# Performance work log

Hardware: AMD Instinct MI355X
Metric: run time of the kernel (lower is better)

## Reference

```python
import jax, jax.numpy as jnp
import numpy as np

B, L, D = 4, 2048, 64
N_HEAD = 4
LOCALITY = 0.2
PI = 3.141592653589793


def setup_inputs() -> dict:
    key = jax.random.key(0)
    k1, k2, k3 = jax.random.split(key, 3)
    mesh = jax.random.uniform(k1, (B, L, 2), dtype=jnp.float32)
    inputs = jax.random.normal(k2, (B, L, D), dtype=jnp.float32)
    lmda = jax.random.uniform(k3, (N_HEAD, 1, 1), dtype=jnp.float32)
    return {"mesh": mesh, "inputs": inputs, "lmda": lmda}


def reference(mesh, inputs, lmda):
    FMAX = jnp.finfo(jnp.float32).max
    # pairwise squared distances: (B, L, L)
    diff = mesh[:, :, None, :] - mesh[:, None, :, :]
    m_dist = jnp.sum(diff * diff, axis=-1)
    # per-head scale in (0, inf): tan(pi/4 * (1-eps) * (1 + sin(lmda)))
    scale = jnp.tan(0.25 * PI * (1.0 - 1e-07) * (1.0 + jnp.sin(lmda)))  # (H,1,1)
    scaled = m_dist[:, None, :, :] * scale  # (B, H, L, L)
    # row-wise quantile threshold (linear interpolation, matching torch.quantile)
    thresh = jnp.quantile(scaled, LOCALITY, axis=-1, keepdims=True)  # (B,H,L,1)
    masked = jnp.where(scaled <= thresh, scaled, FMAX)
    att = jax.nn.softmax(-masked, axis=-1)  # (B, H, L, L)
    # aggregate: (B,H,L,L) x (B,L,D) -> (B,L,H,D) -> (B,L,H*D)
    conv = jnp.einsum('bhnj,bjd->bnhd', att, inputs)
    conv = conv.reshape(inputs.shape[0], -1, N_HEAD * inputs.shape[-1])
    return jnp.concatenate([inputs, conv], axis=-1)
```

## Files before the change

kernel.cpp:

```cpp
#include <hip/hip_runtime.h>
#include <math.h>

#ifndef M_PI
#define M_PI 3.14159265358979323846
#endif

namespace {
constexpr int B_ = 4;
constexpr int L_ = 2048;
constexpr int D_ = 64;
constexpr int H_ = 4;
constexpr int RB = 8;
constexpr int KT = 64;
constexpr int NTILE = L_ / KT;
constexpr int CAPC = 256;
constexpr int OUTW = D_ + H_ * D_;
}

typedef __attribute__((ext_vector_type(8))) short bf16x8;
typedef __attribute__((ext_vector_type(4))) float f32x4;

__device__ __forceinline__ unsigned bf16_rne(float x) {
    unsigned u = __float_as_uint(x);
    return (u + 0x7fffu + ((u >> 16) & 1u)) >> 16;
}

__device__ __forceinline__ unsigned cvt_pk_bf16(float lo, float hi) {
    unsigned r;
    asm("v_cvt_pk_bf16_f32 %0, %1, %2" : "=v"(r) : "v"(lo), "v"(hi));
    return r;
}

#if defined(__has_builtin)
#if __has_builtin(__builtin_amdgcn_exp2f)
#define EXP2F(x) __builtin_amdgcn_exp2f(x)
#endif
#endif
#ifndef EXP2F
#define EXP2F(x) __expf((x) * 0.69314718055994531f)
#endif

#define LDS_FENCE() __builtin_amdgcn_s_waitcnt(0xC07F)

__global__ __launch_bounds__(256) void prep_thresh_kernel(
    const float* __restrict__ mesh,
    const float* __restrict__ inputs,
    char* __restrict__ ws,
    float* __restrict__ out)
{
    __shared__ unsigned s_hist[4][256];
    __shared__ float s_cand[4][256];

    const int t = threadIdx.x;
    const int l = t & 63;
    const int w = t >> 6;
    const int blk = blockIdx.x;

    if (t < 128) {
        const unsigned u = (unsigned)blk * 128u + (unsigned)t;
        const int pb = u >> 16;
        const int rem = u & 65535;
        const int tile = rem >> 12;
        const int idx = rem & 4095;
        const int n = idx & 63;
        const int kl = (idx >> 6) << 1;
        const float* inb = inputs + ((size_t)pb * L_ + tile * 128) * D_;
        char* wsb = ws + (size_t)pb * (L_ * D_ * 2) + tile * (128 * D_ * 2);
        const float x0 = inb[kl * D_ + n];
        const float x1 = inb[(kl + 1) * D_ + n];
        const int chunk = (kl >> 3) * 64 + n;
        const int e = kl & 7;
        *reinterpret_cast<unsigned*>(wsb + chunk * 16 + e * 2) =
            bf16_rne(x0) | (bf16_rne(x1) << 16);
    }

    const int row = blk * 4 + w;
    const int b = row >> 11;
    const int rl = row & 2047;
    const float2* meshg = reinterpret_cast<const float2*>(mesh) + (size_t)b * L_;
    unsigned* hw = s_hist[w];
    float* cw = s_cand[w];
    const float2 me = meshg[rl];

    *reinterpret_cast<uint4*>(&hw[l * 4]) = make_uint4(0u, 0u, 0u, 0u);
    LDS_FENCE();
    #pragma unroll 4
    for (int it = 0; it < 32; ++it) {
        const int j = (it << 6) + l;
        const float2 mj = meshg[j];
        const float dx = __fsub_rn(me.x, mj.x);
        const float dy = __fsub_rn(me.y, mj.y);
        const float d = __fadd_rn(__fmul_rn(dx, dx), __fmul_rn(dy, dy));
        int bin = (int)(d * 128.0f); bin = bin < 255 ? bin : 255;
        atomicAdd(&hw[bin], 1u);
    }
    LDS_FENCE();
    int lo, hi; unsigned base;
    {
        const uint4 hv = *reinterpret_cast<const uint4*>(&hw[l * 4]);
        const unsigned p0 = hv.x, p1 = p0 + hv.y, p2 = p1 + hv.z, p3 = p2 + hv.w;
        unsigned sc = p3;
        #pragma unroll
        for (int off = 1; off < 64; off <<= 1) {
            const unsigned uu = __shfl_up(sc, off);
            if (l >= off) sc += uu;
        }
        const unsigned eb = sc - p3;
        const unsigned cum[4] = {eb + p0, eb + p1, eb + p2, eb + p3};
        int flo = -1, fhi = -1; unsigned fbase = 0u;
        #pragma unroll
        for (int e = 0; e < 4; ++e) {
            const unsigned prev = e ? cum[e - 1] : eb;
            if (cum[e] > 409u && prev <= 409u) { flo = l * 4 + e; fbase = prev; }
            if (cum[e] > 410u && prev <= 410u) { fhi = l * 4 + e; }
        }
        const unsigned long long bmlo = __ballot(flo >= 0);
        const int srclo = (int)__builtin_ctzll(bmlo);
        lo = __shfl(flo, srclo);
        base = __shfl(fbase, srclo);
        const unsigned long long bmhi = __ballot(fhi >= 0);
        hi = __shfl(fhi, (int)__builtin_ctzll(bmhi));
    }
    unsigned cbase = 0u;
    #pragma unroll 4
    for (int it = 0; it < 32; ++it) {
        const int j = (it << 6) + l;
        const float2 mj = meshg[j];
        const float dx = __fsub_rn(me.x, mj.x);
        const float dy = __fsub_rn(me.y, mj.y);
        const float d = __fadd_rn(__fmul_rn(dx, dx), __fmul_rn(dy, dy));
        int bin = (int)(d * 128.0f); bin = bin < 255 ? bin : 255;
        const bool pred = (bin >= lo && bin <= hi);
        const unsigned long long bm = __ballot(pred);
        if (pred) {
            const unsigned p = cbase + (unsigned)__popcll(bm & ((1ull << l) - 1ull));
            if (p < (unsigned)CAPC) cw[p] = d;
        }
        cbase += (unsigned)__popcll(bm);
    }
    LDS_FENCE();
    const int m = (int)min(cbase, (unsigned)CAPC);
    const unsigned k409 = 409u - base;
    const unsigned k410 = 410u - base;
    const float lo_edge = (float)lo * 0.0078125f;
    const float sc2 = 32768.0f / (float)(hi - lo + 1);
    *reinterpret_cast<uint4*>(&hw[l * 4]) = make_uint4(0u, 0u, 0u, 0u);
    LDS_FENCE();
    #pragma unroll 2
    for (int ci = l; ci < m; ci += 64) {
        const float v = cw[ci];
        int b2 = (int)(__fmul_rn(__fsub_rn(v, lo_edge), sc2));
        b2 = b2 < 255 ? b2 : 255; b2 = b2 > 0 ? b2 : 0;
        atomicAdd(&hw[b2], 1u);
    }
    LDS_FENCE();
    int lo2, hi2; unsigned base2;
    {
        const uint4 hv = *reinterpret_cast<const uint4*>(&hw[l * 4]);
        const unsigned p0 = hv.x, p1 = p0 + hv.y, p2 = p1 + hv.z, p3 = p2 + hv.w;
        unsigned sc = p3;
        #pragma unroll
        for (int off = 1; off < 64; off <<= 1) {
            const unsigned uu = __shfl_up(sc, off);
            if (l >= off) sc += uu;
        }
        const unsigned eb = sc - p3;
        const unsigned cum[4] = {eb + p0, eb + p1, eb + p2, eb + p3};
        int flo = -1, fhi = -1; unsigned fbase = 0u;
        #pragma unroll
        for (int e = 0; e < 4; ++e) {
            const unsigned prev = e ? cum[e - 1] : eb;
            if (cum[e] > k409 && prev <= k409) { flo = l * 4 + e; fbase = prev; }
            if (cum[e] > k410 && prev <= k410) { fhi = l * 4 + e; }
        }
        const unsigned long long bmlo = __ballot(flo >= 0);
        const int srclo = (int)__builtin_ctzll(bmlo);
        lo2 = __shfl(flo, srclo);
        base2 = __shfl(fbase, srclo);
        const unsigned long long bmhi = __ballot(fhi >= 0);
        hi2 = __shfl(fhi, (int)__builtin_ctzll(bmhi));
    }
    float* c2 = reinterpret_cast<float*>(hw);
    unsigned cnt2 = 0u;
    for (int c0 = 0; c0 < m; c0 += 64) {
        const int ci = c0 + l;
        float v = 0.0f; bool pred = false;
        if (ci < m) {
            v = cw[ci];
            int b2 = (int)(__fmul_rn(__fsub_rn(v, lo_edge), sc2));
            b2 = b2 < 255 ? b2 : 255; b2 = b2 > 0 ? b2 : 0;
            pred = (b2 >= lo2 && b2 <= hi2);
        }
        const unsigned long long bm = __ballot(pred);
        if (pred) {
            const unsigned p = cnt2 + (unsigned)__popcll(bm & ((1ull << l) - 1ull));
            if (p < 256u) c2[p] = v;
        }
        cnt2 += (unsigned)__popcll(bm);
    }
    LDS_FENCE();
    const int c = (int)min(cnt2, 256u);
    const int q409 = (int)(k409 - base2);
    const int q410 = (int)(k410 - base2);
    if (l == 0) { cw[0] = 0.0f; cw[1] = 0.0f; }
    LDS_FENCE();
    #pragma unroll 1
    for (int cc0 = 0; cc0 < c; cc0 += 64) {
        const int ci = cc0 + l;
        const float v = (ci < c) ? c2[ci] : 0.0f;
        int lt = 0, le = 0;
        #pragma unroll 4
        for (int i = 0; i < c; ++i) {
            const float u = c2[i];
            lt += (u < v) ? 1 : 0;
            le += (u <= v) ? 1 : 0;
        }
        if (ci < c) {
            if (lt <= q409 && q409 < le) cw[0] = v;
            if (lt <= q410 && q410 < le) cw[1] = v;
        }
    }
    LDS_FENCE();
    if (l == 0) {
        const float d409 = cw[0], d410 = cw[1];
        const float pos = 0.2f * 2047.0f;
        const float g = pos - 409.0f;
        const float lw = 1.0f - g;
        const float thD = __fadd_rn(__fmul_rn(d409, lw), __fmul_rn(d410, g));
        out[(size_t)(b * L_ + rl) * OUTW + 319] = thD;
    }
}

__global__ __launch_bounds__(256, 4) void posatt_kernel(
    const float* __restrict__ mesh,
    const float* __restrict__ inputs,
    const float* __restrict__ lmda,
    const char* __restrict__ ws,
    float* __restrict__ out)
{
    __shared__ float s_C[32 * 64];
    __shared__ float s_scale[H_];
    __shared__ float s_thD[RB];
    __shared__ float s_ws2[2][2][16];

    const int t = threadIdx.x;
    const int l = t & 63;
    const int w = t >> 6;
    const int p_w  = w >> 1;
    const int ks_w = w & 1;

    const int blk = blockIdx.x;
    const int xcd = blk & 7;
    const int b = xcd >> 1;
    const int n0 = (((xcd & 1) << 7) + (blk >> 3)) * RB;

    const float2* meshg = reinterpret_cast<const float2*>(mesh) + (size_t)b * L_;

    if (t < H_) {
        const double lam = (double)lmda[t];
        const float C = (float)(0.25 * M_PI * (1.0 - 1e-07));
        const float s1 = (float)sin(lam);
        const float arg = __fmul_rn(C, __fadd_rn(1.0f, s1));
        s_scale[t] = (float)tan((double)arg);
    }
    if (t < RB) {
        s_thD[t] = out[(size_t)(b * L_ + n0 + t) * OUTW + 319];
    }
    __syncthreads();

    const int row16 = l & 15;
    const int kq = l >> 4;
    const int rl = row16 & 7;
    const float2 me = meshg[n0 + rl];
    const float thD = s_thD[rl];
    constexpr float LOG2E = 1.4426950408889634f;
    const float cH = __fmul_rn(-LOG2E, s_scale[p_w * 2 + (row16 >> 3)]);

    const char* bptr = ws + (size_t)b * (L_ * D_ * 2)
                     + ((size_t)(((ks_w * 4 + kq) * 64) + row16) << 4);
    const float4* mptr = reinterpret_cast<const float4*>(meshg) + (ks_w * 16 + kq * 4);

    f32x4 acc[4];
    acc[0] = (f32x4)0.0f; acc[1] = (f32x4)0.0f;
    acc[2] = (f32x4)0.0f; acc[3] = (f32x4)0.0f;
    float wacc = 0.0f;

    uint4 cb0, cb1, cb2, cb3;
    float4 cm0, cm1, cm2, cm3;
    auto LOADT = [&](int tl, uint4& B0, uint4& B1, uint4& B2, uint4& B3,
                     float4& M0, float4& M1, float4& M2, float4& M3) {
        const char* p = bptr + ((size_t)tl << 13);
        B0 = *reinterpret_cast<const uint4*>(p);
        B1 = *reinterpret_cast<const uint4*>(p + 256);
        B2 = *reinterpret_cast<const uint4*>(p + 512);
        B3 = *reinterpret_cast<const uint4*>(p + 768);
        const float4* q = mptr + tl * 32;
        M0 = q[0]; M1 = q[1]; M2 = q[2]; M3 = q[3];
    };
    auto DW = [&](float mx, float my) -> float {
        const float dx = __fsub_rn(me.x, mx);
        const float dy = __fsub_rn(me.y, my);
        const float d = __fadd_rn(__fmul_rn(dx, dx), __fmul_rn(dy, dy));
        const float x = __fmul_rn(d, cH);
        return (d <= thD) ? EXP2F(x) : 0.0f;
    };
    auto STEP = [&]() {
        const float w0 = DW(cm0.x, cm0.y), w1 = DW(cm0.z, cm0.w);
        const float w2 = DW(cm1.x, cm1.y), w3 = DW(cm1.z, cm1.w);
        const float w4 = DW(cm2.x, cm2.y), w5 = DW(cm2.z, cm2.w);
        const float w6 = DW(cm3.x, cm3.y), w7 = DW(cm3.z, cm3.w);
        wacc = __fadd_rn(wacc,
            __fadd_rn(__fadd_rn(__fadd_rn(w0, w1), __fadd_rn(w2, w3)),
                      __fadd_rn(__fadd_rn(w4, w5), __fadd_rn(w6, w7))));
        union { uint4 u; bf16x8 v; } av;
        av.u = make_uint4(cvt_pk_bf16(w0, w1), cvt_pk_bf16(w2, w3),
                          cvt_pk_bf16(w4, w5), cvt_pk_bf16(w6, w7));
        union { uint4 u; bf16x8 v; } b0v, b1v, b2v, b3v;
        b0v.u = cb0; b1v.u = cb1; b2v.u = cb2; b3v.u = cb3;
        acc[0] = __builtin_amdgcn_mfma_f32_16x16x32_bf16(av.v, b0v.v, acc[0], 0, 0, 0);
        acc[1] = __builtin_amdgcn_mfma_f32_16x16x32_bf16(av.v, b1v.v, acc[1], 0, 0, 0);
        acc[2] = __builtin_amdgcn_mfma_f32_16x16x32_bf16(av.v, b2v.v, acc[2], 0, 0, 0);
        acc[3] = __builtin_amdgcn_mfma_f32_16x16x32_bf16(av.v, b3v.v, acc[3], 0, 0, 0);
    };

    LOADT(0, cb0, cb1, cb2, cb3, cm0, cm1, cm2, cm3);
    #pragma unroll 1
    for (int tl = 0; tl < NTILE - 1; ++tl) {
        uint4 nb0, nb1, nb2, nb3;
        float4 nm0, nm1, nm2, nm3;
        LOADT(tl + 1, nb0, nb1, nb2, nb3, nm0, nm1, nm2, nm3);
        STEP();
        cb0 = nb0; cb1 = nb1; cb2 = nb2; cb3 = nb3;
        cm0 = nm0; cm1 = nm1; cm2 = nm2; cm3 = nm3;
    }
    STEP();

    wacc += __shfl_xor(wacc, 16);
    wacc += __shfl_xor(wacc, 32);
    if (l < 16) s_ws2[ks_w][p_w][l] = wacc;
    {
        float4* Cz = reinterpret_cast<float4*>(s_C);
        Cz[t] = make_float4(0.f, 0.f, 0.f, 0.f);
        Cz[t + 256] = make_float4(0.f, 0.f, 0.f, 0.f);
    }
    __syncthreads();
    #pragma unroll
    for (int nq = 0; nq < 4; ++nq) {
        #pragma unroll
        for (int reg = 0; reg < 4; ++reg) {
            const int row = kq * 4 + reg;
            const int col = nq * 16 + row16;
            atomicAdd(&s_C[(p_w * 16 + row) * 64 + col], acc[nq][reg]);
        }
    }
    __syncthreads();
    const float* inpb = inputs + (size_t)b * L_ * D_;
    #pragma unroll
    for (int half = 0; half < 2; ++half) {
        const int s = t + half * 256;
        const int pr = s >> 4;
        const int p = pr >> 4;
        const int r16 = pr & 15;
        const int h = p * 2 + (r16 >> 3);
        const int r = r16 & 7;
        const int col = (s & 15) << 2;
        const float wsv = s_ws2[0][p][r16] + s_ws2[1][p][r16];
        const float inv = (wsv != 0.0f) ? 1.0f / wsv : 0.0f;
        float4 r0 = *reinterpret_cast<const float4*>(&s_C[pr * 64 + col]);
        r0.x *= inv; r0.y *= inv; r0.z *= inv; r0.w *= inv;
        float* op = out + (size_t)(b * L_ + n0 + r) * OUTW + D_ + h * 64 + col;
        *reinterpret_cast<float4*>(op) = r0;
        const int rr2 = s >> 6;
        const int cc2 = s & 63;
        out[(size_t)(b * L_ + n0 + rr2) * OUTW + cc2] =
            inpb[(size_t)(n0 + rr2) * D_ + cc2];
    }
}

extern "C" void kernel_launch(void* const* d_in, const int* in_sizes, int n_in,
                              void* d_out, int out_size, void* d_ws, size_t ws_size,
                              hipStream_t stream) {
    const float* mesh   = (const float*)d_in[0];
    const float* inputs = (const float*)d_in[1];
    const float* lmda   = (const float*)d_in[2];
    float* out = (float*)d_out;
    char* ws = (char*)d_ws;
    (void)in_sizes; (void)n_in; (void)out_size; (void)ws_size;
    hipLaunchKernelGGL(prep_thresh_kernel, dim3(2048), dim3(256), 0, stream,
                       mesh, inputs, ws, out);
    hipLaunchKernelGGL(posatt_kernel, dim3(B_ * (L_ / RB)), dim3(256), 0, stream,
                       mesh, inputs, lmda, ws, out);
}
```

Baseline: 127.0 us.

## Compute all heads per wave with 16-row blocks and LDS-staged mesh

Restructures the attention kernel so each block handles 16 query rows, and each wave processes all four heads over a quarter of the key tiles. The distance computation and B-tile loads are then reused across heads instead of being repeated per head-pair wave. Mesh coordinates for the batch are staged in LDS, B tiles are double-buffered in registers, the block-to-row mapping changes, and the inputs copy uses float4. This raises register pressure (launch bounds drop to 2 blocks per SIMD) and halves the grid, which may reduce occupancy and latency hiding.

Result: slower. 141.4 us (+11.3%).

```diff
diff --git a/kernel.cpp b/kernel.cpp
--- a/kernel.cpp
+++ b/kernel.cpp
@@ -10,9 +10,8 @@
 constexpr int L_ = 2048;
 constexpr int D_ = 64;
 constexpr int H_ = 4;
-constexpr int RB = 8;
-constexpr int KT = 64;
-constexpr int NTILE = L_ / KT;
+constexpr int RB = 16;
+constexpr int NTILE = 32;
 constexpr int CAPC = 256;
 constexpr int OUTW = D_ + H_ * D_;
 }
@@ -231,28 +230,26 @@
     }
 }
 
-__global__ __launch_bounds__(256, 4) void posatt_kernel(
+__global__ __launch_bounds__(256, 2) void posatt_kernel(
     const float* __restrict__ mesh,
     const float* __restrict__ inputs,
     const float* __restrict__ lmda,
     const char* __restrict__ ws,
     float* __restrict__ out)
 {
-    __shared__ float s_C[32 * 64];
+    __shared__ __align__(16) char s_mem[16384];
     __shared__ float s_scale[H_];
     __shared__ float s_thD[RB];
-    __shared__ float s_ws2[2][2][16];
+    __shared__ float s_wsumW[4][H_][RB];
 
     const int t = threadIdx.x;
     const int l = t & 63;
     const int w = t >> 6;
-    const int p_w  = w >> 1;
-    const int ks_w = w & 1;
 
     const int blk = blockIdx.x;
-    const int xcd = blk & 7;
-    const int b = xcd >> 1;
-    const int n0 = (((xcd & 1) << 7) + (blk >> 3)) * RB;
+    const int b = (blk >> 6) & 3;
+    const int rbk = ((blk >> 8) << 6) | (blk & 63);
+    const int n0 = rbk * RB;
 
     const float2* meshg = reinterpret_cast<const float2*>(mesh) + (size_t)b * L_;
 
@@ -266,114 +263,157 @@
     if (t < RB) {
         s_thD[t] = out[(size_t)(b * L_ + n0 + t) * OUTW + 319];
     }
+    {
+        const float4* mg4 = reinterpret_cast<const float4*>(meshg);
+        float4* sm4 = reinterpret_cast<float4*>(s_mem);
+        #pragma unroll
+        for (int i = 0; i < 4; ++i) sm4[t + i * 256] = mg4[t + i * 256];
+    }
     __syncthreads();
 
-    const int row16 = l & 15;
+    const int rr = l & 15;
     const int kq = l >> 4;
-    const int rl = row16 & 7;
-    const float2 me = meshg[n0 + rl];
-    const float thD = s_thD[rl];
+    const float2 me = meshg[n0 + rr];
+    const float thD = s_thD[rr];
     constexpr float LOG2E = 1.4426950408889634f;
-    const float cH = __fmul_rn(-LOG2E, s_scale[p_w * 2 + (row16 >> 3)]);
-
-    const char* bptr = ws + (size_t)b * (L_ * D_ * 2)
-                     + ((size_t)(((ks_w * 4 + kq) * 64) + row16) << 4);
-    const float4* mptr = reinterpret_cast<const float4*>(meshg) + (ks_w * 16 + kq * 4);
-
-    f32x4 acc[4];
-    acc[0] = (f32x4)0.0f; acc[1] = (f32x4)0.0f;
-    acc[2] = (f32x4)0.0f; acc[3] = (f32x4)0.0f;
-    float wacc = 0.0f;
-
-    uint4 cb0, cb1, cb2, cb3;
-    float4 cm0, cm1, cm2, cm3;
-    auto LOADT = [&](int tl, uint4& B0, uint4& B1, uint4& B2, uint4& B3,
-                     float4& M0, float4& M1, float4& M2, float4& M3) {
-        const char* p = bptr + ((size_t)tl << 13);
-        B0 = *reinterpret_cast<const uint4*>(p);
-        B1 = *reinterpret_cast<const uint4*>(p + 256);
-        B2 = *reinterpret_cast<const uint4*>(p + 512);
-        B3 = *reinterpret_cast<const uint4*>(p + 768);
-        const float4* q = mptr + tl * 32;
-        M0 = q[0]; M1 = q[1]; M2 = q[2]; M3 = q[3];
+    float cH[H_];
+    #pragma unroll
+    for (int h = 0; h < H_; ++h) cH[h] = __fmul_rn(-LOG2E, s_scale[h]);
+
+    const char* blane = ws + (size_t)b * (L_ * D_ * 2) + ((kq * 64 + rr) << 4);
+    const float4* smesh4 = reinterpret_cast<const float4*>(s_mem) + (kq << 2);
+
+    f32x4 acc[H_][4];
+    #pragma unroll
+    for (int h = 0; h < H_; ++h)
+        #pragma unroll
+        for (int nq = 0; nq < 4; ++nq) acc[h][nq] = (f32x4)0.0f;
+    float wacc[H_] = {0.f, 0.f, 0.f, 0.f};
+
+    auto LOADB = [&](int tl, uint4 (&Bv)[8]) {
+        const char* p = blane + (size_t)tl * 8192;
+        #pragma unroll
+        for (int s = 0; s < 2; ++s)
+            #pragma unroll
+            for (int nq = 0; nq < 4; ++nq)
+                Bv[s * 4 + nq] = *reinterpret_cast<const uint4*>(
+                    p + s * 4096 + nq * 256);
     };
-    auto DW = [&](float mx, float my) -> float {
+    auto DIST = [&](float mx, float my) -> float {
         const float dx = __fsub_rn(me.x, mx);
         const float dy = __fsub_rn(me.y, my);
-        const float d = __fadd_rn(__fmul_rn(dx, dx), __fmul_rn(dy, dy));
-        const float x = __fmul_rn(d, cH);
-        return (d <= thD) ? EXP2F(x) : 0.0f;
+        return __fadd_rn(__fmul_rn(dx, dx), __fmul_rn(dy, dy));
     };
-    auto STEP = [&]() {
-        const float w0 = DW(cm0.x, cm0.y), w1 = DW(cm0.z, cm0.w);
-        const float w2 = DW(cm1.x, cm1.y), w3 = DW(cm1.z, cm1.w);
-        const float w4 = DW(cm2.x, cm2.y), w5 = DW(cm2.z, cm2.w);
-        const float w6 = DW(cm3.x, cm3.y), w7 = DW(cm3.z, cm3.w);
-        wacc = __fadd_rn(wacc,
-            __fadd_rn(__fadd_rn(__fadd_rn(w0, w1), __fadd_rn(w2, w3)),
-                      __fadd_rn(__fadd_rn(w4, w5), __fadd_rn(w6, w7))));
-        union { uint4 u; bf16x8 v; } av;
-        av.u = make_uint4(cvt_pk_bf16(w0, w1), cvt_pk_bf16(w2, w3),
-                          cvt_pk_bf16(w4, w5), cvt_pk_bf16(w6, w7));
-        union { uint4 u; bf16x8 v; } b0v, b1v, b2v, b3v;
-        b0v.u = cb0; b1v.u = cb1; b2v.u = cb2; b3v.u = cb3;
-        acc[0] = __builtin_amdgcn_mfma_f32_16x16x32_bf16(av.v, b0v.v, acc[0], 0, 0, 0);
-        acc[1] = __builtin_amdgcn_mfma_f32_16x16x32_bf16(av.v, b1v.v, acc[1], 0, 0, 0);
-        acc[2] = __builtin_amdgcn_mfma_f32_16x16x32_bf16(av.v, b2v.v, acc[2], 0, 0, 0);
-        acc[3] = __builtin_amdgcn_mfma_f32_16x16x32_bf16(av.v, b3v.v, acc[3], 0, 0, 0);
+    auto COMPUTE = [&](int tl, const uint4 (&Bv)[8]) {
+        #pragma unroll
+        for (int s = 0; s < 2; ++s) {
+            const float4* mq = smesh4 + (tl * 32 + s * 16);
+            const float4 m0 = mq[0], m1 = mq[1], m2 = mq[2], m3 = mq[3];
+            float d[8];
+            d[0] = DIST(m0.x, m0.y); d[1] = DIST(m0.z, m0.w);
+            d[2] = DIST(m1.x, m1.y); d[3] = DIST(m1.z, m1.w);
+            d[4] = DIST(m2.x, m2.y); d[5] = DIST(m2.z, m2.w);
+            d[6] = DIST(m3.x, m3.y); d[7] = DIST(m3.z, m3.w);
+            #pragma unroll
+            for (int h = 0; h < H_; ++h) {
+                float wv[8];
+                #pragma unroll
+                for (int e = 0; e < 8; ++e) {
+                    const float x = __fmul_rn(d[e], cH[h]);
+                    wv[e] = (d[e] <= thD) ? EXP2F(x) : 0.0f;
+                }
+                wacc[h] = __fadd_rn(wacc[h],
+                    __fadd_rn(__fadd_rn(__fadd_rn(wv[0], wv[1]),
+                                        __fadd_rn(wv[2], wv[3])),
+                              __fadd_rn(__fadd_rn(wv[4], wv[5]),
+                                        __fadd_rn(wv[6], wv[7]))));
+                union { uint4 u; bf16x8 v; } av;
+                av.u = make_uint4(cvt_pk_bf16(wv[0], wv[1]),
+                                  cvt_pk_bf16(wv[2], wv[3]),
+                                  cvt_pk_bf16(wv[4], wv[5]),
+                                  cvt_pk_bf16(wv[6], wv[7]));
+                #pragma unroll
+                for (int nq = 0; nq < 4; ++nq) {
+                    union { uint4 u; bf16x8 v; } bv;
+                    bv.u = Bv[s * 4 + nq];
+                    acc[h][nq] = __builtin_amdgcn_mfma_f32_16x16x32_bf16(
+                        av.v, bv.v, acc[h][nq], 0, 0, 0);
+                }
+            }
+        }
     };
 
-    LOADT(0, cb0, cb1, cb2, cb3, cm0, cm1, cm2, cm3);
+    uint4 bufA[8], bufB[8];
+    LOADB(w, bufA);
     #pragma unroll 1
-    for (int tl = 0; tl < NTILE - 1; ++tl) {
-        uint4 nb0, nb1, nb2, nb3;
-        float4 nm0, nm1, nm2, nm3;
-        LOADT(tl + 1, nb0, nb1, nb2, nb3, nm0, nm1, nm2, nm3);
-        STEP();
-        cb0 = nb0; cb1 = nb1; cb2 = nb2; cb3 = nb3;
-        cm0 = nm0; cm1 = nm1; cm2 = nm2; cm3 = nm3;
-    }
-    STEP();
-
-    wacc += __shfl_xor(wacc, 16);
-    wacc += __shfl_xor(wacc, 32);
-    if (l < 16) s_ws2[ks_w][p_w][l] = wacc;
-    {
-        float4* Cz = reinterpret_cast<float4*>(s_C);
-        Cz[t] = make_float4(0.f, 0.f, 0.f, 0.f);
-        Cz[t + 256] = make_float4(0.f, 0.f, 0.f, 0.f);
-    }
+    for (int i = 0; i < 3; ++i) {
+        LOADB(w + 4 * (2 * i + 1), bufB);
+        COMPUTE(w + 4 * (2 * i), bufA);
+        LOADB(w + 4 * (2 * i + 2), bufA);
+        COMPUTE(w + 4 * (2 * i + 1), bufB);
+    }
+    LOADB(w + 28, bufB);
+    COMPUTE(w + 24, bufA);
+    COMPUTE(w + 28, bufB);
+
+    #pragma unroll
+    for (int h = 0; h < H_; ++h) {
+        wacc[h] += __shfl_xor(wacc[h], 16);
+        wacc[h] += __shfl_xor(wacc[h], 32);
+    }
+    if (l < RB) {
+        #pragma unroll
+        for (int h = 0; h < H_; ++h) s_wsumW[w][h][l] = wacc[h];
+    }
+
     __syncthreads();
-    #pragma unroll
-    for (int nq = 0; nq < 4; ++nq) {
-        #pragma unroll
-        for (int reg = 0; reg < 4; ++reg) {
-            const int row = kq * 4 + reg;
-            const int col = nq * 16 + row16;
-            atomicAdd(&s_C[(p_w * 16 + row) * 64 + col], acc[nq][reg]);
-        }
+    {
+        float4* Cz = reinterpret_cast<float4*>(s_mem);
+        #pragma unroll
+        for (int i = 0; i < 4; ++i)
+            Cz[t + i * 256] = make_float4(0.f, 0.f, 0.f, 0.f);
     }
     __syncthreads();
-    const float* inpb = inputs + (size_t)b * L_ * D_;
-    #pragma unroll
-    for (int half = 0; half < 2; ++half) {
-        const int s = t + half * 256;
-        const int pr = s >> 4;
-        const int p = pr >> 4;
-        const int r16 = pr & 15;
-        const int h = p * 2 + (r16 >> 3);
-        const int r = r16 & 7;
-        const int col = (s & 15) << 2;
-        const float wsv = s_ws2[0][p][r16] + s_ws2[1][p][r16];
-        const float inv = (wsv != 0.0f) ? 1.0f / wsv : 0.0f;
-        float4 r0 = *reinterpret_cast<const float4*>(&s_C[pr * 64 + col]);
-        r0.x *= inv; r0.y *= inv; r0.z *= inv; r0.w *= inv;
-        float* op = out + (size_t)(b * L_ + n0 + r) * OUTW + D_ + h * 64 + col;
-        *reinterpret_cast<float4*>(op) = r0;
-        const int rr2 = s >> 6;
-        const int cc2 = s & 63;
-        out[(size_t)(b * L_ + n0 + rr2) * OUTW + cc2] =
-            inpb[(size_t)(n0 + rr2) * D_ + cc2];
+    {
+        float* Cf = reinterpret_cast<float*>(s_mem);
+        #pragma unroll
+        for (int h = 0; h < H_; ++h)
+            #pragma unroll
+            for (int nq = 0; nq < 4; ++nq)
+                #pragma unroll
+                for (int reg = 0; reg < 4; ++reg) {
+                    const int mrow = kq * 4 + reg;
+                    const int col = nq * 16 + rr;
+                    atomicAdd(&Cf[(h * 16 + mrow) * 64 + col], acc[h][nq][reg]);
+                }
+    }
+    __syncthreads();
+    {
+        const float* Cf = reinterpret_cast<const float*>(s_mem);
+        #pragma unroll
+        for (int q = 0; q < 4; ++q) {
+            const int s = t + q * 256;
+            const int pr = s >> 4;
+            const int h = pr >> 4;
+            const int mrow = pr & 15;
+            const int col = (s & 15) << 2;
+            const float wsv = ((s_wsumW[0][h][mrow] + s_wsumW[1][h][mrow]) +
+                               (s_wsumW[2][h][mrow] + s_wsumW[3][h][mrow]));
+            const float inv = (wsv != 0.0f) ? 1.0f / wsv : 0.0f;
+            float4 r0 = *reinterpret_cast<const float4*>(&Cf[pr * 64 + col]);
+            r0.x *= inv; r0.y *= inv; r0.z *= inv; r0.w *= inv;
+            float* op = out + (size_t)(b * L_ + n0 + mrow) * OUTW + D_ + h * 64 + col;
+            *reinterpret_cast<float4*>(op) = r0;
+        }
+    }
+    {
+        const float* inpb = inputs + (size_t)b * L_ * D_;
+        const int r = t >> 4;
+        const int c = (t & 15) << 2;
+        const float4 v = *reinterpret_cast<const float4*>(
+            &inpb[(size_t)(n0 + r) * D_ + c]);
+        *reinterpret_cast<float4*>(
+            &out[(size_t)(b * L_ + n0 + r) * OUTW + c]) = v;
     }
 }
 
```
